# Kernel tuning notes

Hardware: AMD Instinct MI355X
Metric: run time of the kernel (lower is better)

## Reference

```python
import jax, jax.numpy as jnp
import numpy as np

B, S, D, H = 2, 2048, 1024, 16
HD = D // H  # head_dim = 64


def setup_inputs() -> dict:
    key = jax.random.key(0)
    ks = jax.random.split(key, 12)
    s = 1.0 / np.sqrt(D)
    return {
        "q": jax.random.normal(ks[0], (B, S, D), jnp.float32),
        "k": jax.random.normal(ks[1], (B, S, D), jnp.float32),
        "v": jax.random.normal(ks[2], (B, S, D), jnp.float32),
        "mask": jnp.zeros((B, 1, 1, S), jnp.float32),
        "wq": jax.random.normal(ks[3], (D, D), jnp.float32) * s,
        "bq": jnp.zeros((D,), jnp.float32),
        "wk": jax.random.normal(ks[4], (D, D), jnp.float32) * s,
        "bk": jnp.zeros((D,), jnp.float32),
        "wv": jax.random.normal(ks[5], (D, D), jnp.float32) * s,
        "bv": jnp.zeros((D,), jnp.float32),
        "wo": jax.random.normal(ks[6], (D, D), jnp.float32) * s,
        "bo": jnp.zeros((D,), jnp.float32),
    }


def _split_heads(x):
    # [B, S, D] -> [B, H, S, HD]
    return x.reshape(B, S, H, HD).transpose(0, 2, 1, 3)


def reference(q, k, v, mask, wq, bq, wk, bk, wv, bv, wo, bo):
    _q = _split_heads(q @ wq + bq)
    _k = _split_heads(k @ wk + bk)
    _v = _split_heads(v @ wv + bv)
    scale = jnp.sqrt(jnp.float32(HD)) + 1e-8
    score = jnp.einsum("bhqd,bhkd->bhqk", _q, _k) / scale
    score = score + mask * -1e9
    attn = jax.nn.softmax(score, axis=-1)
    ctx = jnp.einsum("bhqk,bhkd->bhqd", attn, _v)
    ctx = ctx.transpose(0, 2, 1, 3).reshape(B, S, D)
    # dropout is identity at inference (training=False)
    return ctx @ wo + bo
```

## Files before the change

### kernel.cpp

```cpp
#include <hip/hip_runtime.h>
#include <hip/hip_bf16.h>

typedef unsigned short u16;
typedef __attribute__((ext_vector_type(8))) short s16x8;
typedef __attribute__((ext_vector_type(4))) short s16x4;
typedef __attribute__((ext_vector_type(4))) float f32x4;
typedef __attribute__((ext_vector_type(8))) unsigned short u16x8;
typedef __attribute__((ext_vector_type(4))) unsigned int u32x4;

#define AS1(p) (const __attribute__((address_space(1))) void*)(p)
#define AS3(p) (__attribute__((address_space(3))) void*)(p)

__device__ __forceinline__ u16 f2bf(float f) {
  unsigned u = __builtin_bit_cast(unsigned, f);
  u += 0x7fffu + ((u >> 16) & 1u);
  return (u16)(u >> 16);
}

__device__ __forceinline__ unsigned cvtpk(float lo, float hi) {
  unsigned r;
  asm("v_cvt_pk_bf16_f32 %0, %1, %2" : "=v"(r) : "v"(lo), "v"(hi));
  return r;
}

__global__ __launch_bounds__(256) void prep(const float* __restrict__ q,
                                            const float* __restrict__ k,
                                            const float* __restrict__ v,
                                            const float* __restrict__ wq,
                                            const float* __restrict__ wk,
                                            const float* __restrict__ wv,
                                            const float* __restrict__ wo,
                                            u16* __restrict__ Xq, u16* __restrict__ Xk,
                                            u16* __restrict__ Xv, u16* __restrict__ Wqt,
                                            u16* __restrict__ Wkt, u16* __restrict__ Wvt,
                                            u16* __restrict__ Wot) {
  __shared__ float t[32][33];
  const int bid = blockIdx.x, tid = threadIdx.x;
  if (bid < 6144) {
    const int m = bid >> 11;
    const float* in = m == 0 ? q : m == 1 ? k : v;
    u16* out = m == 0 ? Xq : m == 1 ? Xk : Xv;
    const int i = ((bid & 2047) * 256 + tid) * 8;
    f32x4 a = *(const f32x4*)(in + i);
    f32x4 b = *(const f32x4*)(in + i + 4);
    u16x8 r;
    r[0] = f2bf(a[0]); r[1] = f2bf(a[1]); r[2] = f2bf(a[2]); r[3] = f2bf(a[3]);
    r[4] = f2bf(b[0]); r[5] = f2bf(b[1]); r[6] = f2bf(b[2]); r[7] = f2bf(b[3]);
    *(u16x8*)(out + i) = r;
  } else {
    const int b2 = bid - 6144;
    const int wsel = b2 >> 10;
    const float* w = wsel == 0 ? wq : wsel == 1 ? wk : wsel == 2 ? wv : wo;
    u16* wt = wsel == 0 ? Wqt : wsel == 1 ? Wkt : wsel == 2 ? Wvt : Wot;
    const int n0 = (b2 & 31) * 32, k0 = ((b2 >> 5) & 31) * 32;
    const int tx = tid & 31, ty = tid >> 5;
#pragma unroll
    for (int i = 0; i < 4; i++)
      t[ty + 8 * i][tx] = w[(size_t)(k0 + ty + 8 * i) * 1024 + n0 + tx];
    __syncthreads();
#pragma unroll
    for (int i = 0; i < 4; i++)
      wt[(size_t)(n0 + ty + 8 * i) * 1024 + k0 + tx] = f2bf(t[tx][ty + 8 * i]);
  }
}

__global__ __launch_bounds__(256) void gemm_qkv(const u16* __restrict__ Xq,
                                                const u16* __restrict__ Xk,
                                                const u16* __restrict__ Xv,
                                                const u16* __restrict__ Wqt,
                                                const u16* __restrict__ Wkt,
                                                const u16* __restrict__ Wvt,
                                                const float* __restrict__ bq,
                                                const float* __restrict__ bk,
                                                const float* __restrict__ bv,
                                                u16* __restrict__ Qb, u16* __restrict__ Kb,
                                                u16* __restrict__ Vt) {
  const int mode = blockIdx.z;
  const u16* A = mode == 0 ? Xq : mode == 1 ? Xk : Xv;
  const u16* Bt = mode == 0 ? Wqt : mode == 1 ? Wkt : Wvt;
  const float* bias = mode == 0 ? bq : mode == 1 ? bk : bv;
  u16* outp = mode == 0 ? Qb : mode == 1 ? Kb : Vt;

  __shared__ u16 Als[128 * 64];
  __shared__ u16 Bls[128 * 64];
  const int tid = threadIdx.x;
  const int lane = tid & 63;
  const int wid = tid >> 6;
  const int wm = wid >> 1, wn = wid & 1;
  const int m0 = blockIdx.y * 128, n0 = blockIdx.x * 128;
  const int g = lane >> 4, c = lane & 15;
  const int srl = lane >> 3, sch0 = lane & 7;
  f32x4 acc[4][4] = {};
  for (int kk = 0; kk < 1024; kk += 64) {
    __syncthreads();
#pragma unroll
    for (int j = 0; j < 4; j++) {
      const int rl = wid * 32 + j * 8 + srl;
      const int col = kk + ((sch0 ^ (rl & 7)) << 3);
      __builtin_amdgcn_global_load_lds(AS1(A + (size_t)(m0 + rl) * 1024 + col),
                                       AS3(&Als[(wid * 32 + j * 8) * 64]), 16, 0, 0);
      __builtin_amdgcn_global_load_lds(AS1(Bt + (size_t)(n0 + rl) * 1024 + col),
                                       AS3(&Bls[(wid * 32 + j * 8) * 64]), 16, 0, 0);
    }
    __syncthreads();
#pragma unroll
    for (int half = 0; half < 2; half++) {
      s16x8 af[4], bfr[4];
#pragma unroll
      for (int mi = 0; mi < 4; mi++) {
        const int r = wm * 64 + mi * 16 + c;
        af[mi] = *(const s16x8*)&Als[r * 64 + (((half * 4 + g) ^ (r & 7)) << 3)];
      }
#pragma unroll
      for (int ni = 0; ni < 4; ni++) {
        const int r = wn * 64 + ni * 16 + c;
        bfr[ni] = *(const s16x8*)&Bls[r * 64 + (((half * 4 + g) ^ (r & 7)) << 3)];
      }
      __builtin_amdgcn_s_setprio(1);
#pragma unroll
      for (int mi = 0; mi < 4; mi++)
#pragma unroll
        for (int ni = 0; ni < 4; ni++)
          acc[mi][ni] = __builtin_amdgcn_mfma_f32_16x16x32_bf16(af[mi], bfr[ni],
                                                                acc[mi][ni], 0, 0, 0);
      __builtin_amdgcn_s_setprio(0);
    }
  }
#pragma unroll
  for (int mi = 0; mi < 4; mi++) {
#pragma unroll
    for (int ni = 0; ni < 4; ni++) {
      const int gn = n0 + wn * 64 + ni * 16 + c;
      const float bb = bias[gn];
      const int gmb = m0 + wm * 64 + mi * 16 + (g << 2);
      const int hd = gn >> 6, d = gn & 63;
      if (mode == 2) {
        const int b = gmb >> 11, s0 = gmb & 2047;
        const int tile = s0 >> 6;
        const int jb = gmb & 63;
        const int j5b = jb & 31;
        const int posb = ((jb >> 5) << 5) + (((j5b & 15) >> 2) << 3) + ((j5b >> 4) << 2);
        s16x4 st;
#pragma unroll
        for (int r = 0; r < 4; r++) st[r] = (short)f2bf(acc[mi][ni][r] + bb);
        *(s16x4*)&Vt[(((size_t)b * 16 + hd) * 64 + d) * 2048 + tile * 64 + posb] = st;
      } else {
#pragma unroll
        for (int r = 0; r < 4; r++) {
          const int gm = gmb + r;
          float val = acc[mi][ni][r] + bb;
          const int b = gm >> 11, s = gm & 2047;
          if (mode == 0) val *= 0.18033688f;
          outp[(((size_t)b * 16 + hd) * 2048 + s) * 64 + d] = f2bf(val);
        }
      }
    }
  }
}

__global__ __launch_bounds__(256) void gemm_out(const u16* __restrict__ A,
                                                const u16* __restrict__ Bt,
                                                const float* __restrict__ bias,
                                                float* __restrict__ outp) {
  __shared__ u16 Als[128 * 64];
  __shared__ u16 Bls[64 * 64];
  const int tid = threadIdx.x;
  const int lane = tid & 63;
  const int wid = tid >> 6;
  const int m0 = blockIdx.y * 128, n0 = blockIdx.x * 64;
  const int g = lane >> 4, c = lane & 15;
  const int srl = lane >> 3, sch0 = lane & 7;
  f32x4 acc[2][4] = {};
  for (int kk = 0; kk < 1024; kk += 64) {
    __syncthreads();
#pragma unroll
    for (int j = 0; j < 4; j++) {
      const int rl = wid * 32 + j * 8 + srl;
      const int col = kk + ((sch0 ^ (rl & 7)) << 3);
      __builtin_amdgcn_global_load_lds(AS1(A + (size_t)(m0 + rl) * 1024 + col),
                                       AS3(&Als[(wid * 32 + j * 8) * 64]), 16, 0, 0);
    }
#pragma unroll
    for (int j = 0; j < 2; j++) {
      const int rl = wid * 16 + j * 8 + srl;
      const int col = kk + ((sch0 ^ (rl & 7)) << 3);
      __builtin_amdgcn_global_load_lds(AS1(Bt + (size_t)(n0 + rl) * 1024 + col),
                                       AS3(&Bls[(wid * 16 + j * 8) * 64]), 16, 0, 0);
    }
    __syncthreads();
#pragma unroll
    for (int half = 0; half < 2; half++) {
      s16x8 af[2], bfr[4];
#pragma unroll
      for (int mi = 0; mi < 2; mi++) {
        const int r = wid * 32 + mi * 16 + c;
        af[mi] = *(const s16x8*)&Als[r * 64 + (((half * 4 + g) ^ (r & 7)) << 3)];
      }
#pragma unroll
      for (int ni = 0; ni < 4; ni++) {
        const int r = ni * 16 + c;
        bfr[ni] = *(const s16x8*)&Bls[r * 64 + (((half * 4 + g) ^ (r & 7)) << 3)];
      }
      __builtin_amdgcn_s_setprio(1);
#pragma unroll
      for (int mi = 0; mi < 2; mi++)
#pragma unroll
        for (int ni = 0; ni < 4; ni++)
          acc[mi][ni] = __builtin_amdgcn_mfma_f32_16x16x32_bf16(af[mi], bfr[ni],
                                                                acc[mi][ni], 0, 0, 0);
      __builtin_amdgcn_s_setprio(0);
    }
  }
#pragma unroll
  for (int mi = 0; mi < 2; mi++) {
#pragma unroll
    for (int ni = 0; ni < 4; ni++) {
      const int gn = n0 + ni * 16 + c;
      const float bb = bias[gn];
      const int gmb = m0 + wid * 32 + mi * 16 + (g << 2);
#pragma unroll
      for (int r = 0; r < 4; r++)
        outp[(size_t)(gmb + r) * 1024 + gn] = acc[mi][ni][r] + bb;
    }
  }
}

__global__ __launch_bounds__(128) void attn_fwd(const u16* __restrict__ Qb,
                                                const u16* __restrict__ Kb,
                                                const u16* __restrict__ Vt,
                                                const float* __restrict__ mask,
                                                u16* __restrict__ ctx) {
  __shared__ u16 Kls[2][4096];
  __shared__ u16 Vls[2][4096];
  const int tid = threadIdx.x;
  const int lane = tid & 63, wid = tid >> 6;
  const int n = blockIdx.x;
  const int bh = ((n & 7) << 2) | ((n >> 3) & 3);
  const int qblk = n >> 5;
  const int b = bh >> 4, hd = bh & 15;
  const int g = lane >> 4, c = lane & 15;
  const int qbase = qblk * 64 + wid * 32;

  s16x8 qf[2][2];
#pragma unroll
  for (int sub = 0; sub < 2; sub++) {
    const u16* Qp = Qb + ((size_t)bh * 2048 + qbase + sub * 16 + c) * 64;
    qf[sub][0] = *(const s16x8*)(Qp + g * 8);
    qf[sub][1] = *(const s16x8*)(Qp + 32 + g * 8);
  }

  const u16* Kbh = Kb + (size_t)bh * 2048 * 64;
  const u16* Vbh = Vt + (size_t)bh * 64 * 2048;
  const float* mp = mask + (size_t)b * 2048;

  const int srl = lane >> 3;
  const int sch0 = lane & 7;
  auto STAGE = [&](int kv0, int bufi) {
#pragma unroll
    for (int j = 0; j < 4; j++) {
      const int rl = wid * 32 + j * 8 + srl;
      const int sch = sch0 ^ (rl & 7);
      __builtin_amdgcn_global_load_lds(AS1(Kbh + (size_t)(kv0 + rl) * 64 + sch * 8),
                                       AS3(&Kls[bufi][wid * 2048 + j * 512]), 16, 0, 0);
      __builtin_amdgcn_global_load_lds(AS1(Vbh + (size_t)rl * 2048 + kv0 + sch * 8),
                                       AS3(&Vls[bufi][wid * 2048 + j * 512]), 16, 0, 0);
    }
  };

  f32x4 o[2][4] = {};
  f32x4 ts2[2] = {};

  STAGE(0, 0);
  int buf = 0;
  for (int t = 0; t < 32; t++) {
    const int kv0 = t * 64;
    __syncthreads();
    if (t < 31) STAGE(kv0 + 64, buf ^ 1);

    f32x4 sacc[2][4] = {};
    __builtin_amdgcn_s_setprio(1);
#pragma unroll
    for (int kvt = 0; kvt < 4; kvt++) {
      const int row = kvt * 16 + c;
      const int s7 = row & 7;
      const s16x8 kf0 = *(const s16x8*)&Kls[buf][row * 64 + ((g ^ s7) << 3)];
      const s16x8 kf1 = *(const s16x8*)&Kls[buf][row * 64 + (((4 + g) ^ s7) << 3)];
      sacc[0][kvt] = __builtin_amdgcn_mfma_f32_16x16x32_bf16(kf0, qf[0][0], sacc[0][kvt], 0, 0, 0);
      sacc[0][kvt] = __builtin_amdgcn_mfma_f32_16x16x32_bf16(kf1, qf[0][1], sacc[0][kvt], 0, 0, 0);
      sacc[1][kvt] = __builtin_amdgcn_mfma_f32_16x16x32_bf16(kf0, qf[1][0], sacc[1][kvt], 0, 0, 0);
      sacc[1][kvt] = __builtin_amdgcn_mfma_f32_16x16x32_bf16(kf1, qf[1][1], sacc[1][kvt], 0, 0, 0);
    }
    __builtin_amdgcn_s_setprio(0);

    f32x4 mk[4];
#pragma unroll
    for (int kvt = 0; kvt < 4; kvt++)
      mk[kvt] = *(const f32x4*)(mp + kv0 + kvt * 16 + 4 * g);

    s16x8 pf[2][2];
#pragma unroll
    for (int qs = 0; qs < 2; qs++) {
      f32x4 p4[4];
#pragma unroll
      for (int kvt = 0; kvt < 4; kvt++) {
#pragma unroll
        for (int j = 0; j < 4; j++)
          p4[kvt][j] = __builtin_amdgcn_exp2f(fmaf(mk[kvt][j], -1.44269504e9f,
                                                   sacc[qs][kvt][j]));
        ts2[qs] += p4[kvt];
      }
#pragma unroll
      for (int sub = 0; sub < 2; sub++) {
        u32x4 ww;
        ww[0] = cvtpk(p4[sub * 2][0], p4[sub * 2][1]);
        ww[1] = cvtpk(p4[sub * 2][2], p4[sub * 2][3]);
        ww[2] = cvtpk(p4[sub * 2 + 1][0], p4[sub * 2 + 1][1]);
        ww[3] = cvtpk(p4[sub * 2 + 1][2], p4[sub * 2 + 1][3]);
        pf[qs][sub] = __builtin_bit_cast(s16x8, ww);
      }
    }

    __builtin_amdgcn_s_setprio(1);
#pragma unroll
    for (int dblk = 0; dblk < 4; dblk++) {
      const int row = dblk * 16 + c;
      const int s7 = row & 7;
      const u16* base = &Vls[buf][row * 64];
#pragma unroll
      for (int subk = 0; subk < 2; subk++) {
        const s16x8 vf = *(const s16x8*)(base + (((subk * 4 + g) ^ s7) << 3));
        o[0][dblk] = __builtin_amdgcn_mfma_f32_16x16x32_bf16(vf, pf[0][subk], o[0][dblk], 0, 0, 0);
        o[1][dblk] = __builtin_amdgcn_mfma_f32_16x16x32_bf16(vf, pf[1][subk], o[1][dblk], 0, 0, 0);
      }
    }
    __builtin_amdgcn_s_setprio(0);
    buf ^= 1;
  }

#pragma unroll
  for (int qs = 0; qs < 2; qs++) {
    float ts = (ts2[qs][0] + ts2[qs][1]) + (ts2[qs][2] + ts2[qs][3]);
    ts += __shfl_xor(ts, 16);
    ts += __shfl_xor(ts, 32);
    const float inv = 1.0f / ts;
    u16* cp = ctx + ((size_t)b * 2048 + qbase + qs * 16 + c) * 1024 + hd * 64;
#pragma unroll
    for (int d = 0; d < 4; d++)
#pragma unroll
      for (int r = 0; r < 4; r++)
        cp[d * 16 + 4 * g + r] = f2bf(o[qs][d][r] * inv);
  }
}

extern "C" void kernel_launch(void* const* d_in, const int* in_sizes, int n_in,
                              void* d_out, int out_size, void* d_ws, size_t ws_size,
                              hipStream_t stream) {
  (void)in_sizes; (void)n_in; (void)out_size; (void)ws_size;
  const float* q = (const float*)d_in[0];
  const float* k = (const float*)d_in[1];
  const float* v = (const float*)d_in[2];
  const float* mask = (const float*)d_in[3];
  const float* wq = (const float*)d_in[4];
  const float* bq = (const float*)d_in[5];
  const float* wk = (const float*)d_in[6];
  const float* bk = (const float*)d_in[7];
  const float* wv = (const float*)d_in[8];
  const float* bv = (const float*)d_in[9];
  const float* wo = (const float*)d_in[10];
  const float* bo = (const float*)d_in[11];
  float* out = (float*)d_out;
  char* ws = (char*)d_ws;
  const size_t MB = (size_t)1 << 20;
  u16* Xq = (u16*)(ws + 0 * MB);
  u16* Xk = (u16*)(ws + 8 * MB);
  u16* Xv = (u16*)(ws + 16 * MB);
  u16* Wqt = (u16*)(ws + 24 * MB);
  u16* Wkt = (u16*)(ws + 26 * MB);
  u16* Wvt = (u16*)(ws + 28 * MB);
  u16* Wot = (u16*)(ws + 30 * MB);
  u16* Qb = (u16*)(ws + 32 * MB);
  u16* Kb = (u16*)(ws + 40 * MB);
  u16* Vt = (u16*)(ws + 48 * MB);
  u16* ctx = Xq;

  prep<<<10240, 256, 0, stream>>>(q, k, v, wq, wk, wv, wo, Xq, Xk, Xv, Wqt, Wkt, Wvt, Wot);
  gemm_qkv<<<dim3(8, 32, 3), 256, 0, stream>>>(Xq, Xk, Xv, Wqt, Wkt, Wvt, bq, bk, bv,
                                               Qb, Kb, Vt);
  attn_fwd<<<1024, 128, 0, stream>>>(Qb, Kb, Vt, mask, ctx);
  gemm_out<<<dim3(16, 32), 256, 0, stream>>>(ctx, Wot, bo, out);
}
```

Baseline: 138.9 us.

## Deepen KV prefetch pipeline, preload scaled mask to LDS, vectorize ctx stores

Restructures the attention loop to keep two KV tiles in flight. It waits with explicit vmcnt counts instead of a full __syncthreads, loads V fragments into registers early, and issues the next-next tile's stage after a mid-iteration barrier. The mask is premultiplied and staged into LDS once per block, which removes per-iteration global mask loads and an FMA. Output stores become packed bf16 pairs. Risks are hand-tuned waitcnt correctness, extra register pressure from holding V fragments, and removal of the setprio hints.

```diff
diff --git a/kernel.cpp b/kernel.cpp
--- a/kernel.cpp
+++ b/kernel.cpp
@@ -7,6 +7,7 @@
 typedef __attribute__((ext_vector_type(4))) float f32x4;
 typedef __attribute__((ext_vector_type(8))) unsigned short u16x8;
 typedef __attribute__((ext_vector_type(4))) unsigned int u32x4;
+typedef __attribute__((ext_vector_type(2))) unsigned int u32x2;
 
 #define AS1(p) (const __attribute__((address_space(1))) void*)(p)
 #define AS3(p) (__attribute__((address_space(3))) void*)(p)
@@ -232,6 +233,7 @@
                                                 u16* __restrict__ ctx) {
   __shared__ u16 Kls[2][4096];
   __shared__ u16 Vls[2][4096];
+  __shared__ float Mls[2048];
   const int tid = threadIdx.x;
   const int lane = tid & 63, wid = tid >> 6;
   const int n = blockIdx.x;
@@ -241,6 +243,15 @@
   const int g = lane >> 4, c = lane & 15;
   const int qbase = qblk * 64 + wid * 32;
 
+  const float* mp = mask + (size_t)b * 2048;
+#pragma unroll
+  for (int i = 0; i < 4; i++) {
+    const int idx = (i * 128 + tid) * 4;
+    f32x4 m4 = *(const f32x4*)(mp + idx);
+    m4 *= -1.44269504e9f;
+    *(f32x4*)&Mls[idx] = m4;
+  }
+
   s16x8 qf[2][2];
 #pragma unroll
   for (int sub = 0; sub < 2; sub++) {
@@ -251,7 +262,6 @@
 
   const u16* Kbh = Kb + (size_t)bh * 2048 * 64;
   const u16* Vbh = Vt + (size_t)bh * 64 * 2048;
-  const float* mp = mask + (size_t)b * 2048;
 
   const int srl = lane >> 3;
   const int sch0 = lane & 7;
@@ -271,14 +281,22 @@
   f32x4 ts2[2] = {};
 
   STAGE(0, 0);
-  int buf = 0;
+  STAGE(64, 1);
+  asm volatile("s_waitcnt lgkmcnt(0)" ::: "memory");
+
   for (int t = 0; t < 32; t++) {
     const int kv0 = t * 64;
-    __syncthreads();
-    if (t < 31) STAGE(kv0 + 64, buf ^ 1);
+    const int buf = t & 1;
+    if (t < 31) {
+      asm volatile("s_waitcnt vmcnt(8)" ::: "memory");
+    } else {
+      asm volatile("s_waitcnt vmcnt(0)" ::: "memory");
+    }
+    __builtin_amdgcn_sched_barrier(0);
+    __builtin_amdgcn_s_barrier();
+    __builtin_amdgcn_sched_barrier(0);
 
     f32x4 sacc[2][4] = {};
-    __builtin_amdgcn_s_setprio(1);
 #pragma unroll
     for (int kvt = 0; kvt < 4; kvt++) {
       const int row = kvt * 16 + c;
@@ -290,12 +308,21 @@
       sacc[1][kvt] = __builtin_amdgcn_mfma_f32_16x16x32_bf16(kf0, qf[1][0], sacc[1][kvt], 0, 0, 0);
       sacc[1][kvt] = __builtin_amdgcn_mfma_f32_16x16x32_bf16(kf1, qf[1][1], sacc[1][kvt], 0, 0, 0);
     }
-    __builtin_amdgcn_s_setprio(0);
-
-    f32x4 mk[4];
-#pragma unroll
-    for (int kvt = 0; kvt < 4; kvt++)
-      mk[kvt] = *(const f32x4*)(mp + kv0 + kvt * 16 + 4 * g);
+
+    s16x8 vreg[4][2];
+#pragma unroll
+    for (int dblk = 0; dblk < 4; dblk++) {
+      const int row = dblk * 16 + c;
+      const int s7 = row & 7;
+      const u16* base = &Vls[buf][row * 64];
+      vreg[dblk][0] = *(const s16x8*)(base + ((g ^ s7) << 3));
+      vreg[dblk][1] = *(const s16x8*)(base + (((4 + g) ^ s7) << 3));
+    }
+    asm volatile("s_waitcnt lgkmcnt(0)" ::: "memory");
+    __builtin_amdgcn_sched_barrier(0);
+    __builtin_amdgcn_s_barrier();
+    __builtin_amdgcn_sched_barrier(0);
+    if (t < 30) STAGE(kv0 + 128, buf);
 
     s16x8 pf[2][2];
 #pragma unroll
@@ -303,10 +330,10 @@
       f32x4 p4[4];
 #pragma unroll
       for (int kvt = 0; kvt < 4; kvt++) {
+        const f32x4 mk = *(const f32x4*)&Mls[kv0 + kvt * 16 + 4 * g];
 #pragma unroll
         for (int j = 0; j < 4; j++)
-          p4[kvt][j] = __builtin_amdgcn_exp2f(fmaf(mk[kvt][j], -1.44269504e9f,
-                                                   sacc[qs][kvt][j]));
+          p4[kvt][j] = __builtin_amdgcn_exp2f(sacc[qs][kvt][j] + mk[j]);
         ts2[qs] += p4[kvt];
       }
 #pragma unroll
@@ -320,21 +347,13 @@
       }
     }
 
-    __builtin_amdgcn_s_setprio(1);
-#pragma unroll
-    for (int dblk = 0; dblk < 4; dblk++) {
-      const int row = dblk * 16 + c;
-      const int s7 = row & 7;
-      const u16* base = &Vls[buf][row * 64];
+#pragma unroll
+    for (int dblk = 0; dblk < 4; dblk++)
 #pragma unroll
       for (int subk = 0; subk < 2; subk++) {
-        const s16x8 vf = *(const s16x8*)(base + (((subk * 4 + g) ^ s7) << 3));
-        o[0][dblk] = __builtin_amdgcn_mfma_f32_16x16x32_bf16(vf, pf[0][subk], o[0][dblk], 0, 0, 0);
-        o[1][dblk] = __builtin_amdgcn_mfma_f32_16x16x32_bf16(vf, pf[1][subk], o[1][dblk], 0, 0, 0);
-      }
-    }
-    __builtin_amdgcn_s_setprio(0);
-    buf ^= 1;
+        o[0][dblk] = __builtin_amdgcn_mfma_f32_16x16x32_bf16(vreg[dblk][subk], pf[0][subk], o[0][dblk], 0, 0, 0);
+        o[1][dblk] = __builtin_amdgcn_mfma_f32_16x16x32_bf16(vreg[dblk][subk], pf[1][subk], o[1][dblk], 0, 0, 0);
+      }
   }
 
 #pragma unroll
@@ -345,10 +364,12 @@
     const float inv = 1.0f / ts;
     u16* cp = ctx + ((size_t)b * 2048 + qbase + qs * 16 + c) * 1024 + hd * 64;
 #pragma unroll
-    for (int d = 0; d < 4; d++)
-#pragma unroll
-      for (int r = 0; r < 4; r++)
-        cp[d * 16 + 4 * g + r] = f2bf(o[qs][d][r] * inv);
+    for (int d = 0; d < 4; d++) {
+      u32x2 st;
+      st[0] = cvtpk(o[qs][d][0] * inv, o[qs][d][1] * inv);
+      st[1] = cvtpk(o[qs][d][2] * inv, o[qs][d][3] * inv);
+      *(u32x2*)&cp[d * 16 + 4 * g] = st;
+    }
   }
 }
 
```

Result: no change. 137.2 us (-1.2%).
